# Kernel optimization log

Hardware: AMD Instinct MI355X
Metric: run time of the kernel (lower is better)

## Reference

```python
import jax, jax.numpy as jnp
import numpy as np


def setup_inputs() -> dict:
    key = jax.random.key(0)
    k1, k2, k3, k4, k5 = jax.random.split(key, 5)
    B, T, H, E, F = 4, 2048, 2048, 8, 1024
    s_h = 1.0 / np.sqrt(H)
    s_f = 1.0 / np.sqrt(F)
    return {
        "hidden_states": jax.random.normal(k1, (B, T, H), dtype=jnp.float32),
        "W_router": jax.random.normal(k2, (H, E), dtype=jnp.float32) * s_h,
        "W_gate": jax.random.normal(k3, (E, H, F), dtype=jnp.float32) * s_h,
        "W_up": jax.random.normal(k4, (E, H, F), dtype=jnp.float32) * s_h,
        "W_down": jax.random.normal(k5, (E, F, H), dtype=jnp.float32) * s_f,
    }


def reference(hidden_states, W_router, W_gate, W_up, W_down):
    B, T, H = hidden_states.shape
    E = W_router.shape[1]
    x = hidden_states.reshape(-1, H)  # [N, H]
    # ReMoE router: linear -> ReLU, non-negative weights per expert
    weights = jax.nn.relu(x @ W_router)  # [N, E]
    # Per-expert SwiGLU FFN applied to all tokens; zero-weight experts
    # contribute exactly zero, matching the original masked dispatch.
    gate = jnp.einsum('nh,ehf->enf', x, W_gate)  # [E, N, F]
    up = jnp.einsum('nh,ehf->enf', x, W_up)      # [E, N, F]
    hid = jax.nn.silu(gate) * up                 # [E, N, F]
    expert_out = jnp.einsum('enf,efh->enh', hid, W_down)  # [E, N, H]
    out_flat = jnp.einsum('ne,enh->nh', weights, expert_out)  # [N, H]
    out = out_flat.reshape(B, T, H)
    router_weights = weights.reshape(B, T, E)
    return (out, router_weights)
```

## Files before the change

### kernel.cpp

```cpp
#include <hip/hip_runtime.h>
#include <hip/hip_bf16.h>

#define N_TOK 8192
#define HD    2048
#define NE    8
#define FF    1024

using f32x4  = __attribute__((ext_vector_type(4))) float;
using bf16x8 = __attribute__((ext_vector_type(8))) __bf16;

__device__ __forceinline__ unsigned short f2bf(float f) {
  unsigned u = __float_as_uint(f);
  u += 0x7FFFu + ((u >> 16) & 1u);
  return (unsigned short)(u >> 16);
}

__device__ __forceinline__ void gl_lds16(const void* g, void* l) {
  __builtin_amdgcn_global_load_lds((__attribute__((address_space(1))) void*)g,
                                   (__attribute__((address_space(3))) void*)l,
                                   16, 0, 0);
}

__device__ __forceinline__ void stage256(const unsigned short* g, size_t lda, int k0,
                                         char* slotbase, int wv, int sr8, int scol) {
  #pragma unroll
  for (int c = 0; c < 4; ++c) {
    const int grp = c * 8 + wv;
    gl_lds16(g + (size_t)(grp * 8 + sr8) * lda + k0 + scol, slotbase + grp * 1024);
  }
}
__device__ __forceinline__ void stage256i(const unsigned short* const aP[4], int k0,
                                          char* slotbase, int wv) {
  #pragma unroll
  for (int c = 0; c < 4; ++c) {
    const int grp = c * 8 + wv;
    gl_lds16(aP[c] + k0, slotbase + grp * 1024);
  }
}
__device__ __forceinline__ void stage128(const unsigned short* g, size_t lda, int k0,
                                         char* slotbase, int wv, int sr8, int scol) {
  #pragma unroll
  for (int c = 0; c < 2; ++c) {
    const int grp = c * 8 + wv;
    gl_lds16(g + (size_t)(grp * 8 + sr8) * lda + k0 + scol, slotbase + grp * 1024);
  }
}

__global__ void k_tconv(const float* __restrict__ in, unsigned short* __restrict__ out,
                        int R, int C, size_t in_z, size_t out_z, size_t ostride) {
  __shared__ float tile[32][33];
  const int z = blockIdx.z;
  const int c0 = blockIdx.x * 32, r0 = blockIdx.y * 32;
  const int tx = threadIdx.x, ty = threadIdx.y;
  const float* ip = in + (size_t)z * in_z;
  unsigned short* op = out + (size_t)z * out_z;
  #pragma unroll
  for (int i = ty; i < 32; i += 8)
    tile[i][tx] = ip[(size_t)(r0 + i) * C + (c0 + tx)];
  __syncthreads();
  #pragma unroll
  for (int i = ty; i < 32; i += 8)
    op[(size_t)(c0 + i) * ostride + (r0 + tx)] = f2bf(tile[tx][i]);
}

__global__ void k_router(const float* __restrict__ x, const float* __restrict__ Wr,
                         float* __restrict__ w, float* __restrict__ rout,
                         unsigned short* __restrict__ xb) {
  const int lane = threadIdx.x & 63, wv = threadIdx.x >> 6;
  const int n = blockIdx.x * 4 + wv;
  const float* xr = x + (size_t)n * HD + lane * 32;
  unsigned short* xbr = xb + (size_t)n * HD + lane * 32;
  const float* wbase = Wr + (size_t)lane * 32 * NE;
  float acc[8];
  #pragma unroll
  for (int e = 0; e < 8; ++e) acc[e] = 0.f;
  #pragma unroll
  for (int kk = 0; kk < 32; kk += 4) {
    float4 xv = *reinterpret_cast<const float4*>(xr + kk);
    ushort4 o;
    o.x = f2bf(xv.x); o.y = f2bf(xv.y); o.z = f2bf(xv.z); o.w = f2bf(xv.w);
    *reinterpret_cast<ushort4*>(xbr + kk) = o;
    #pragma unroll
    for (int t = 0; t < 4; ++t) {
      const float* wrow = wbase + (kk + t) * 8;
      float4 w0 = *reinterpret_cast<const float4*>(wrow);
      float4 w1 = *reinterpret_cast<const float4*>(wrow + 4);
      float xs = (t == 0) ? xv.x : (t == 1) ? xv.y : (t == 2) ? xv.z : xv.w;
      acc[0] += xs * w0.x; acc[1] += xs * w0.y; acc[2] += xs * w0.z; acc[3] += xs * w0.w;
      acc[4] += xs * w1.x; acc[5] += xs * w1.y; acc[6] += xs * w1.z; acc[7] += xs * w1.w;
    }
  }
  #pragma unroll
  for (int off = 32; off; off >>= 1) {
    #pragma unroll
    for (int e = 0; e < 8; ++e) acc[e] += __shfl_down(acc[e], off);
  }
  if (lane == 0) {
    #pragma unroll
    for (int e = 0; e < 8; ++e) {
      float v = acc[e] > 0.f ? acc[e] : 0.f;
      w[n * 8 + e] = v;
      rout[n * 8 + e] = v;
    }
  }
}

__global__ void k_compact(const float* __restrict__ w, int* __restrict__ idx,
                          int* __restrict__ cnt) {
  const int e = blockIdx.x;
  __shared__ int base;
  __shared__ int scan[4];
  if (threadIdx.x == 0) base = 0;
  __syncthreads();
  const int lane = threadIdx.x & 63, wvi = threadIdx.x >> 6;
  for (int c0 = 0; c0 < N_TOK; c0 += 256) {
    const int n = c0 + threadIdx.x;
    const bool act = w[n * 8 + e] > 0.f;
    unsigned long long m = __ballot(act);
    const int pre  = __popcll(m & ((1ull << lane) - 1ull));
    if (lane == 0) scan[wvi] = __popcll(m);
    __syncthreads();
    int woff = 0;
    #pragma unroll
    for (int i = 0; i < 4; ++i) if (i < wvi) woff += scan[i];
    const int tot = scan[0] + scan[1] + scan[2] + scan[3];
    if (act) idx[e * N_TOK + base + woff + pre] = n;
    __syncthreads();
    if (threadIdx.x == 0) base += tot;
    __syncthreads();
  }
  const int M = base;
  if (threadIdx.x == 0) cnt[e] = M;
  const int Mpad = (M + 255) & ~255;
  for (int i = M + threadIdx.x; i < Mpad; i += 256) idx[e * N_TOK + i] = 0;
}

#define G1_PHASE(cpK) do {                                                       \
    const char* Ab_ = As + rs * 32768 + (wr * 64) * 128 + rb;                    \
    const char* Bg_ = Bgs + rs * 16384 + (wc * 64) * 128 + rb;                   \
    const char* Bu_ = Bus + rs * 16384 + (wc * 64) * 128 + rb;                   \
    bf16x8 av_[4], bg_[4], bu_[4];                                               \
    _Pragma("unroll")                                                            \
    for (int i = 0; i < 4; ++i) av_[i] = *(const bf16x8*)(Ab_ + i * 2048 + (cpK)); \
    _Pragma("unroll")                                                            \
    for (int j = 0; j < 4; ++j) {                                                \
      bg_[j] = *(const bf16x8*)(Bg_ + j * 2048 + (cpK));                         \
      bu_[j] = *(const bf16x8*)(Bu_ + j * 2048 + (cpK));                         \
    }                                                                            \
    __builtin_amdgcn_s_setprio(1);                                               \
    _Pragma("unroll")                                                            \
    for (int i = 0; i < 4; ++i) {                                                \
      _Pragma("unroll")                                                          \
      for (int j = 0; j < 4; ++j) {                                              \
        ag[i][j] = __builtin_amdgcn_mfma_f32_16x16x32_bf16(av_[i], bg_[j], ag[i][j], 0,0,0); \
        au[i][j] = __builtin_amdgcn_mfma_f32_16x16x32_bf16(av_[i], bu_[j], au[i][j], 0,0,0); \
      }                                                                          \
    }                                                                            \
    __builtin_amdgcn_s_setprio(0);                                               \
  } while (0)

__global__ void __launch_bounds__(512, 2) k_gemm1(
    const unsigned short* __restrict__ xb,
    const unsigned short* __restrict__ Wg,
    const unsigned short* __restrict__ Wu,
    const float* __restrict__ w,
    const int* __restrict__ idx,
    const int* __restrict__ cnt,
    unsigned short* __restrict__ A2,
    int e0, int k2g, int nwg) {
  extern __shared__ char lds[];
  char* As  = lds;
  char* Bgs = lds + 65536;
  char* Bus = lds + 98304;
  const int tid = threadIdx.x;
  const int l = tid & 63, wv = tid >> 6;

  const int h = blockIdx.x;
  const int chunk = nwg >> 3;
  const int L = (h & 7) * chunk + (h >> 3);
  const int eloc = L >> 8;
  const int e = e0 + eloc;
  const int idxq = L & 255;
  const int sub = idxq >> 5;
  const int f = ((sub & 1) << 2) | ((idxq >> 3) & 3);
  const int y = ((sub >> 1) << 3) | (idxq & 7);
  const int bm = y << 8;
  const int bf = f << 7;
  const int wr = wv >> 1, wc = wv & 1;

  const int Me = cnt[e];
  if (bm >= Me) return;
  const int* idxe = idx + e * N_TOK;

  const unsigned short* gBg = Wg + ((size_t)e * FF + bf) * HD;
  const unsigned short* gBu = Wu + ((size_t)e * FF + bf) * HD;

  const int sr8  = l >> 3;
  const int scol = ((l & 7) ^ sr8) << 3;
  const int fr  = l & 15;
  const int rb  = fr << 7;
  const int kc  = (l >> 4) << 4;
  const int swz = (l & 7) << 4;
  const int cp0 = kc ^ swz;
  const int cp1 = (64 + kc) ^ swz;

  const unsigned short* aP[4];
  #pragma unroll
  for (int c = 0; c < 4; ++c)
    aP[c] = xb + (size_t)idxe[bm + (c * 8 + wv) * 8 + sr8] * HD + scol;

  f32x4 ag[4][4], au[4][4];
  const f32x4 zero = {0.f, 0.f, 0.f, 0.f};
  #pragma unroll
  for (int i = 0; i < 4; ++i) {
    #pragma unroll
    for (int j = 0; j < 4; ++j) { ag[i][j] = zero; au[i][j] = zero; }
  }

  stage256i(aP, 0, As, wv);
  stage128(gBg, HD, 0, Bgs, wv, sr8, scol);
  stage128(gBu, HD, 0, Bus, wv, sr8, scol);
  asm volatile("s_waitcnt vmcnt(0)" ::: "memory");
  __builtin_amdgcn_s_barrier();
  __builtin_amdgcn_sched_barrier(0);

  const int NT = HD / 64;
  for (int t = 0; t < NT; ++t) {
    const int tn = (t + 1 < NT) ? t + 1 : NT - 1;
    const int sw = (t + 1) & 1;
    const int rs = t & 1;
    stage128(gBg, HD, tn * 64, Bgs + sw * 16384, wv, sr8, scol);
    stage128(gBu, HD, tn * 64, Bus + sw * 16384, wv, sr8, scol);
    G1_PHASE(cp0);
    stage256i(aP, tn * 64, As + sw * 32768, wv);
    G1_PHASE(cp1);
    asm volatile("s_waitcnt vmcnt(0)" ::: "memory");
    __builtin_amdgcn_s_barrier();
    __builtin_amdgcn_sched_barrier(0);
  }

  const int orow = (l >> 4) << 2;
  #pragma unroll
  for (int am = 0; am < 4; ++am) {
    #pragma unroll
    for (int rr = 0; rr < 4; ++rr) {
      const int cm = bm + wr * 64 + am * 16 + orow + rr;
      const int n = idxe[cm];
      const float wn = w[n * 8 + e];
      size_t obase = (size_t)n * k2g + (size_t)eloc * FF + bf + wc * 64 + fr;
      #pragma unroll
      for (int j = 0; j < 4; ++j) {
        const float g = ag[am][j][rr];
        const float u = au[am][j][rr];
        const float s = g / (1.f + __expf(-g));
        A2[obase + j * 16] = f2bf(s * u * wn);
      }
    }
  }
}

#define G2_PHASE(cpK) do {                                                       \
    const char* Ab_ = As + rs * 32768 + (wr * 128) * 128 + rb;                   \
    const char* Bb_ = Bs + rs * 32768 + (wc * 64) * 128 + rb;                    \
    bf16x8 av_[8], bv_[4];                                                       \
    _Pragma("unroll")                                                            \
    for (int i = 0; i < 8; ++i) av_[i] = *(const bf16x8*)(Ab_ + i * 2048 + (cpK)); \
    _Pragma("unroll")                                                            \
    for (int j = 0; j < 4; ++j) bv_[j] = *(const bf16x8*)(Bb_ + j * 2048 + (cpK)); \
    __builtin_amdgcn_s_setprio(1);                                               \
    _Pragma("unroll")                                                            \
    for (int i = 0; i < 8; ++i) {                                                \
      _Pragma("unroll")                                                          \
      for (int j = 0; j < 4; ++j)                                                \
        acc[i][j] = __builtin_amdgcn_mfma_f32_16x16x32_bf16(av_[i], bv_[j], acc[i][j], 0,0,0); \
    }                                                                            \
    __builtin_amdgcn_s_setprio(0);                                               \
  } while (0)

__global__ void __launch_bounds__(512, 2) k_gemm2(
    const unsigned short* __restrict__ A2,
    const unsigned short* __restrict__ Wd,
    float* __restrict__ out,
    int k2g, int accum) {
  extern __shared__ char lds[];
  char* As = lds;
  char* Bs = lds + 65536;
  const int tid = threadIdx.x;
  const int l = tid & 63, wv = tid >> 6;

  const int h = blockIdx.x;
  const int L = (h & 7) * 32 + (h >> 3);
  const int y = L >> 3;
  const int x = L & 7;
  const int bm = y << 8;
  const int bn = x << 8;
  const int wr = wv >> 2, wc = wv & 3;

  const unsigned short* gA = A2 + (size_t)bm * k2g;
  const unsigned short* gB = Wd + (size_t)bn * (NE * FF);

  const int sr8  = l >> 3;
  const int scol = ((l & 7) ^ sr8) << 3;
  const int fr  = l & 15;
  const int rb  = fr << 7;
  const int kc  = (l >> 4) << 4;
  const int swz = (l & 7) << 4;
  const int cp0 = kc ^ swz;
  const int cp1 = (64 + kc) ^ swz;

  f32x4 acc[8][4];
  const f32x4 zero = {0.f, 0.f, 0.f, 0.f};
  #pragma unroll
  for (int i = 0; i < 8; ++i) {
    #pragma unroll
    for (int j = 0; j < 4; ++j) acc[i][j] = zero;
  }

  stage256(gA, k2g, 0, As, wv, sr8, scol);
  stage256(gB, NE * FF, 0, Bs, wv, sr8, scol);
  asm volatile("s_waitcnt vmcnt(0)" ::: "memory");
  __builtin_amdgcn_s_barrier();
  __builtin_amdgcn_sched_barrier(0);

  const int NT = k2g / 64;
  for (int t = 0; t < NT; ++t) {
    const int tn = (t + 1 < NT) ? t + 1 : NT - 1;
    const int sw = (t + 1) & 1;
    const int rs = t & 1;
    stage256(gB, NE * FF, tn * 64, Bs + sw * 32768, wv, sr8, scol);
    G2_PHASE(cp0);
    stage256(gA, k2g, tn * 64, As + sw * 32768, wv, sr8, scol);
    G2_PHASE(cp1);
    asm volatile("s_waitcnt vmcnt(0)" ::: "memory");
    __builtin_amdgcn_s_barrier();
    __builtin_amdgcn_sched_barrier(0);
  }

  const int orow = (l >> 4) << 2;
  #pragma unroll
  for (int am = 0; am < 8; ++am) {
    #pragma unroll
    for (int rr = 0; rr < 4; ++rr) {
      const int n = bm + wr * 128 + am * 16 + orow + rr;
      float* op = out + (size_t)n * HD + bn + wc * 64 + fr;
      #pragma unroll
      for (int j = 0; j < 4; ++j) {
        const float v = acc[am][j][rr];
        op[j * 16] = accum ? (op[j * 16] + v) : v;
      }
    }
  }
}

extern "C" void kernel_launch(void* const* d_in, const int* in_sizes, int n_in,
                              void* d_out, int out_size, void* d_ws, size_t ws_size,
                              hipStream_t stream) {
  (void)in_sizes; (void)out_size;
  if (n_in < 5) return;
  const float* x  = (const float*)d_in[0];
  const float* Wr = (const float*)d_in[1];
  const float* Wg = (const float*)d_in[2];
  const float* Wu = (const float*)d_in[3];
  const float* Wd = (const float*)d_in[4];
  float* out  = (float*)d_out;
  float* rout = out + (size_t)N_TOK * HD;

  hipFuncSetAttribute((const void*)k_gemm1, hipFuncAttributeMaxDynamicSharedMemorySize, 131072);
  hipFuncSetAttribute((const void*)k_gemm2, hipFuncAttributeMaxDynamicSharedMemorySize, 131072);

  char* ws = (char*)d_ws;
  const size_t SZ_XB = (size_t)N_TOK * HD * 2;
  const size_t SZ_W  = (size_t)NE * HD * FF * 2;
  unsigned short* xb    = (unsigned short*)(ws);
  unsigned short* Wg_bt = (unsigned short*)(ws + SZ_XB);
  unsigned short* Wu_bt = (unsigned short*)(ws + SZ_XB + SZ_W);
  unsigned short* Wd_bt = (unsigned short*)(ws + SZ_XB + 2 * SZ_W);
  float*          wbuf  = (float*)(ws + SZ_XB + 3 * SZ_W);
  size_t off = SZ_XB + 3 * SZ_W + (size_t)N_TOK * NE * 4;
  int* idxbuf = (int*)(ws + off);  off += (size_t)NE * N_TOK * 4;
  int* cntbuf = (int*)(ws + off);  off += 256;
  const size_t fixed = off;
  unsigned short* A2 = (unsigned short*)(ws + fixed);

  const size_t perE = (size_t)N_TOK * FF * 2;
  int G = 8;
  while (G > 1 && fixed + (size_t)G * perE > ws_size) G >>= 1;

  dim3 tb(32, 8);
  k_tconv<<<dim3(FF / 32, HD / 32, NE), tb, 0, stream>>>(
      Wg, Wg_bt, HD, FF, (size_t)HD * FF, (size_t)FF * HD, (size_t)HD);
  k_tconv<<<dim3(FF / 32, HD / 32, NE), tb, 0, stream>>>(
      Wu, Wu_bt, HD, FF, (size_t)HD * FF, (size_t)FF * HD, (size_t)HD);
  k_tconv<<<dim3(HD / 32, FF / 32, NE), tb, 0, stream>>>(
      Wd, Wd_bt, FF, HD, (size_t)FF * HD, (size_t)FF, (size_t)(NE * FF));

  k_router<<<N_TOK / 4, 256, 0, stream>>>(x, Wr, wbuf, rout, xb);

  k_compact<<<NE, 256, 0, stream>>>(wbuf, idxbuf, cntbuf);

  const int k2g = G * FF;
  for (int e0 = 0; e0 < NE; e0 += G) {
    hipMemsetAsync(A2, 0, (size_t)G * perE, stream);
    const int nwg1 = 256 * G;
    k_gemm1<<<nwg1, 512, 131072, stream>>>(xb, Wg_bt, Wu_bt, wbuf, idxbuf, cntbuf,
                                           A2, e0, k2g, nwg1);
    k_gemm2<<<(N_TOK / 256) * (HD / 256), 512, 131072, stream>>>(
        A2, Wd_bt + (size_t)e0 * FF, out, k2g, e0 != 0);
  }
}
```

Before: 690.4 us.

## Split K tiles into halves with deeper async prefetch and partial waits in both GEMMs

Both expert GEMM kernels now stage each 64-wide K tile as two 32-wide halves in a new swizzled LDS layout. Prefetch runs up to two half-tiles ahead, and the full vmcnt(0) drain is replaced by vmcnt(8) waits with a barrier per half. Global-to-LDS loads are interleaved between MFMA groups to keep more memory traffic in flight and shorten stalls at each barrier. The cost is a second barrier per K step and more intricate buffer-reuse ordering, where a wrong wait count or slot overlap would give a race.

```diff
diff --git a/kernel.cpp b/kernel.cpp
--- a/kernel.cpp
+++ b/kernel.cpp
@@ -21,30 +21,11 @@
                                    16, 0, 0);
 }
 
-__device__ __forceinline__ void stage256(const unsigned short* g, size_t lda, int k0,
-                                         char* slotbase, int wv, int sr8, int scol) {
-  #pragma unroll
-  for (int c = 0; c < 4; ++c) {
-    const int grp = c * 8 + wv;
-    gl_lds16(g + (size_t)(grp * 8 + sr8) * lda + k0 + scol, slotbase + grp * 1024);
-  }
-}
-__device__ __forceinline__ void stage256i(const unsigned short* const aP[4], int k0,
-                                          char* slotbase, int wv) {
-  #pragma unroll
-  for (int c = 0; c < 4; ++c) {
-    const int grp = c * 8 + wv;
-    gl_lds16(aP[c] + k0, slotbase + grp * 1024);
-  }
-}
-__device__ __forceinline__ void stage128(const unsigned short* g, size_t lda, int k0,
-                                         char* slotbase, int wv, int sr8, int scol) {
-  #pragma unroll
-  for (int c = 0; c < 2; ++c) {
-    const int grp = c * 8 + wv;
-    gl_lds16(g + (size_t)(grp * 8 + sr8) * lda + k0 + scol, slotbase + grp * 1024);
-  }
-}
+#define WAIT8_BAR() do {                                      \
+    asm volatile("s_waitcnt vmcnt(8)" ::: "memory");          \
+    __builtin_amdgcn_s_barrier();                             \
+    __builtin_amdgcn_sched_barrier(0);                        \
+  } while (0)
 
 __global__ void k_tconv(const float* __restrict__ in, unsigned short* __restrict__ out,
                         int R, int C, size_t in_z, size_t out_z, size_t ostride) {
@@ -135,28 +116,40 @@
   for (int i = M + threadIdx.x; i < Mpad; i += 256) idx[e * N_TOK + i] = 0;
 }
 
-#define G1_PHASE(cpK) do {                                                       \
-    const char* Ab_ = As + rs * 32768 + (wr * 64) * 128 + rb;                    \
-    const char* Bg_ = Bgs + rs * 16384 + (wc * 64) * 128 + rb;                   \
-    const char* Bu_ = Bus + rs * 16384 + (wc * 64) * 128 + rb;                   \
-    bf16x8 av_[4], bg_[4], bu_[4];                                               \
-    _Pragma("unroll")                                                            \
-    for (int i = 0; i < 4; ++i) av_[i] = *(const bf16x8*)(Ab_ + i * 2048 + (cpK)); \
-    _Pragma("unroll")                                                            \
-    for (int j = 0; j < 4; ++j) {                                                \
-      bg_[j] = *(const bf16x8*)(Bg_ + j * 2048 + (cpK));                         \
-      bu_[j] = *(const bf16x8*)(Bu_ + j * 2048 + (cpK));                         \
-    }                                                                            \
+#define G1_MFMA(accM, barr) do {                                                 \
     __builtin_amdgcn_s_setprio(1);                                               \
     _Pragma("unroll")                                                            \
     for (int i = 0; i < 4; ++i) {                                                \
       _Pragma("unroll")                                                          \
-      for (int j = 0; j < 4; ++j) {                                              \
-        ag[i][j] = __builtin_amdgcn_mfma_f32_16x16x32_bf16(av_[i], bg_[j], ag[i][j], 0,0,0); \
-        au[i][j] = __builtin_amdgcn_mfma_f32_16x16x32_bf16(av_[i], bu_[j], au[i][j], 0,0,0); \
-      }                                                                          \
+      for (int j = 0; j < 4; ++j)                                                \
+        accM[i][j] = __builtin_amdgcn_mfma_f32_16x16x32_bf16(av_[i], (barr)[j], accM[i][j], 0,0,0); \
     }                                                                            \
     __builtin_amdgcn_s_setprio(0);                                               \
+  } while (0)
+
+#define G1_ST_A(koff, base) do {                                                 \
+    gl_lds16(aP0 + (koff), (base) + wv * 1024);                                  \
+    gl_lds16(aP1 + (koff), (base) + (wv + 8) * 1024);                            \
+  } while (0)
+#define G1_ST_B(koff, bgb, bub) do {                                             \
+    gl_lds16(gBg + bOff + (koff), (bgb) + wv * 1024);                            \
+    gl_lds16(gBu + bOff + (koff), (bub) + wv * 1024);                            \
+  } while (0)
+
+#define G1_HALF(rsl, hh, ISSUE_B) do {                                           \
+    const char* Ab_ = As  + (rsl) * 32768 + (hh) * 16384 + aoff;                 \
+    const char* Bg_ = Bgs + (rsl) * 16384 + (hh) * 8192 + boff;                  \
+    const char* Bu_ = Bus + (rsl) * 16384 + (hh) * 8192 + boff;                  \
+    bf16x8 av_[4], bb_[4];                                                       \
+    _Pragma("unroll")                                                            \
+    for (int i = 0; i < 4; ++i) av_[i] = *(const bf16x8*)(Ab_ + i * 1024);       \
+    _Pragma("unroll")                                                            \
+    for (int j = 0; j < 4; ++j) bb_[j] = *(const bf16x8*)(Bg_ + j * 1024);       \
+    G1_MFMA(ag, bb_);                                                            \
+    ISSUE_B;                                                                     \
+    _Pragma("unroll")                                                            \
+    for (int j = 0; j < 4; ++j) bb_[j] = *(const bf16x8*)(Bu_ + j * 1024);       \
+    G1_MFMA(au, bb_);                                                            \
   } while (0)
 
 __global__ void __launch_bounds__(512, 2) k_gemm1(
@@ -195,19 +188,15 @@
   const unsigned short* gBg = Wg + ((size_t)e * FF + bf) * HD;
   const unsigned short* gBu = Wu + ((size_t)e * FF + bf) * HD;
 
-  const int sr8  = l >> 3;
-  const int scol = ((l & 7) ^ sr8) << 3;
+  const int scolE = (((l & 3) ^ ((l >> 3) & 3)) << 3);
   const int fr  = l & 15;
-  const int rb  = fr << 7;
-  const int kc  = (l >> 4) << 4;
-  const int swz = (l & 7) << 4;
-  const int cp0 = kc ^ swz;
-  const int cp1 = (64 + kc) ^ swz;
-
-  const unsigned short* aP[4];
-  #pragma unroll
-  for (int c = 0; c < 4; ++c)
-    aP[c] = xb + (size_t)idxe[bm + (c * 8 + wv) * 8 + sr8] * HD + scol;
+  const int cph = (((l >> 4) ^ ((fr >> 1) & 3)) << 4);
+  const int aoff = (wr * 64 + fr) * 64 + cph;
+  const int boff = (wc * 64 + fr) * 64 + cph;
+
+  const unsigned short* aP0 = xb + (size_t)idxe[bm + wv * 16 + (l >> 2)] * HD + scolE;
+  const unsigned short* aP1 = xb + (size_t)idxe[bm + (wv + 8) * 16 + (l >> 2)] * HD + scolE;
+  const size_t bOff = (size_t)(wv * 16 + (l >> 2)) * HD + scolE;
 
   f32x4 ag[4][4], au[4][4];
   const f32x4 zero = {0.f, 0.f, 0.f, 0.f};
@@ -217,26 +206,25 @@
     for (int j = 0; j < 4; ++j) { ag[i][j] = zero; au[i][j] = zero; }
   }
 
-  stage256i(aP, 0, As, wv);
-  stage128(gBg, HD, 0, Bgs, wv, sr8, scol);
-  stage128(gBu, HD, 0, Bus, wv, sr8, scol);
-  asm volatile("s_waitcnt vmcnt(0)" ::: "memory");
-  __builtin_amdgcn_s_barrier();
-  __builtin_amdgcn_sched_barrier(0);
+  G1_ST_A(0,  As);
+  G1_ST_B(0,  Bgs, Bus);
+  G1_ST_A(32, As + 16384);
+  G1_ST_B(32, Bgs + 8192, Bus + 8192);
+  G1_ST_A(64, As + 32768);
+  G1_ST_B(64, Bgs + 16384, Bus + 16384);
+  WAIT8_BAR();
 
   const int NT = HD / 64;
   for (int t = 0; t < NT; ++t) {
-    const int tn = (t + 1 < NT) ? t + 1 : NT - 1;
-    const int sw = (t + 1) & 1;
-    const int rs = t & 1;
-    stage128(gBg, HD, tn * 64, Bgs + sw * 16384, wv, sr8, scol);
-    stage128(gBu, HD, tn * 64, Bus + sw * 16384, wv, sr8, scol);
-    G1_PHASE(cp0);
-    stage256i(aP, tn * 64, As + sw * 32768, wv);
-    G1_PHASE(cp1);
-    asm volatile("s_waitcnt vmcnt(0)" ::: "memory");
-    __builtin_amdgcn_s_barrier();
-    __builtin_amdgcn_sched_barrier(0);
+    const int rs = t & 1, sw = rs ^ 1;
+    const int kn1 = ((t + 1 < NT) ? t + 1 : NT - 1) * 64;
+    const int kn2 = ((t + 2 < NT) ? t + 2 : NT - 1) * 64;
+    G1_ST_A(kn1 + 32, As + sw * 32768 + 16384);
+    G1_HALF(rs, 0, G1_ST_B(kn1 + 32, Bgs + sw * 16384 + 8192, Bus + sw * 16384 + 8192));
+    WAIT8_BAR();
+    G1_ST_A(kn2, As + rs * 32768);
+    G1_HALF(rs, 1, G1_ST_B(kn2, Bgs + rs * 16384, Bus + rs * 16384));
+    WAIT8_BAR();
   }
 
   const int orow = (l >> 4) << 2;
@@ -259,17 +247,35 @@
   }
 }
 
-#define G2_PHASE(cpK) do {                                                       \
-    const char* Ab_ = As + rs * 32768 + (wr * 128) * 128 + rb;                   \
-    const char* Bb_ = Bs + rs * 32768 + (wc * 64) * 128 + rb;                    \
+#define G2_ST_A(koff, base) do {                                                 \
+    gl_lds16(gA + aOff0 + (koff), (base) + wv * 1024);                           \
+    gl_lds16(gA + aOff1 + (koff), (base) + (wv + 8) * 1024);                     \
+  } while (0)
+#define G2_ST_B(koff, base) do {                                                 \
+    gl_lds16(gB + bOff0 + (koff), (base) + wv * 1024);                           \
+    gl_lds16(gB + bOff1 + (koff), (base) + (wv + 8) * 1024);                     \
+  } while (0)
+
+#define G2_HALF(rsl, hh, ISSUE_B) do {                                           \
+    const char* Ab_ = As + (rsl) * 32768 + (hh) * 16384 + aoff;                  \
+    const char* Bb_ = Bs + (rsl) * 32768 + (hh) * 16384 + boff;                  \
     bf16x8 av_[8], bv_[4];                                                       \
     _Pragma("unroll")                                                            \
-    for (int i = 0; i < 8; ++i) av_[i] = *(const bf16x8*)(Ab_ + i * 2048 + (cpK)); \
-    _Pragma("unroll")                                                            \
-    for (int j = 0; j < 4; ++j) bv_[j] = *(const bf16x8*)(Bb_ + j * 2048 + (cpK)); \
+    for (int i = 0; i < 8; ++i) av_[i] = *(const bf16x8*)(Ab_ + i * 1024);       \
+    _Pragma("unroll")                                                            \
+    for (int j = 0; j < 4; ++j) bv_[j] = *(const bf16x8*)(Bb_ + j * 1024);       \
     __builtin_amdgcn_s_setprio(1);                                               \
     _Pragma("unroll")                                                            \
-    for (int i = 0; i < 8; ++i) {                                                \
+    for (int i = 0; i < 4; ++i) {                                                \
+      _Pragma("unroll")                                                          \
+      for (int j = 0; j < 4; ++j)                                                \
+        acc[i][j] = __builtin_amdgcn_mfma_f32_16x16x32_bf16(av_[i], bv_[j], acc[i][j], 0,0,0); \
+    }                                                                            \
+    __builtin_amdgcn_s_setprio(0);                                               \
+    ISSUE_B;                                                                     \
+    __builtin_amdgcn_s_setprio(1);                                               \
+    _Pragma("unroll")                                                            \
+    for (int i = 4; i < 8; ++i) {                                                \
       _Pragma("unroll")                                                          \
       for (int j = 0; j < 4; ++j)                                                \
         acc[i][j] = __builtin_amdgcn_mfma_f32_16x16x32_bf16(av_[i], bv_[j], acc[i][j], 0,0,0); \
@@ -299,14 +305,16 @@
   const unsigned short* gA = A2 + (size_t)bm * k2g;
   const unsigned short* gB = Wd + (size_t)bn * (NE * FF);
 
-  const int sr8  = l >> 3;
-  const int scol = ((l & 7) ^ sr8) << 3;
+  const int scolE = (((l & 3) ^ ((l >> 3) & 3)) << 3);
   const int fr  = l & 15;
-  const int rb  = fr << 7;
-  const int kc  = (l >> 4) << 4;
-  const int swz = (l & 7) << 4;
-  const int cp0 = kc ^ swz;
-  const int cp1 = (64 + kc) ^ swz;
+  const int cph = (((l >> 4) ^ ((fr >> 1) & 3)) << 4);
+  const int aoff = (wr * 128 + fr) * 64 + cph;
+  const int boff = (wc * 64 + fr) * 64 + cph;
+
+  const size_t aOff0 = (size_t)(wv * 16 + (l >> 2)) * k2g + scolE;
+  const size_t aOff1 = (size_t)((wv + 8) * 16 + (l >> 2)) * k2g + scolE;
+  const size_t bOff0 = (size_t)(wv * 16 + (l >> 2)) * (NE * FF) + scolE;
+  const size_t bOff1 = (size_t)((wv + 8) * 16 + (l >> 2)) * (NE * FF) + scolE;
 
   f32x4 acc[8][4];
   const f32x4 zero = {0.f, 0.f, 0.f, 0.f};
@@ -316,24 +324,25 @@
     for (int j = 0; j < 4; ++j) acc[i][j] = zero;
   }
 
-  stage256(gA, k2g, 0, As, wv, sr8, scol);
-  stage256(gB, NE * FF, 0, Bs, wv, sr8, scol);
-  asm volatile("s_waitcnt vmcnt(0)" ::: "memory");
-  __builtin_amdgcn_s_barrier();
-  __builtin_amdgcn_sched_barrier(0);
+  G2_ST_A(0,  As);
+  G2_ST_B(0,  Bs);
+  G2_ST_A(32, As + 16384);
+  G2_ST_B(32, Bs + 16384);
+  G2_ST_A(64, As + 32768);
+  G2_ST_B(64, Bs + 32768);
+  WAIT8_BAR();
 
   const int NT = k2g / 64;
   for (int t = 0; t < NT; ++t) {
-    const int tn = (t + 1 < NT) ? t + 1 : NT - 1;
-    const int sw = (t + 1) & 1;
-    const int rs = t & 1;
-    stage256(gB, NE * FF, tn * 64, Bs + sw * 32768, wv, sr8, scol);
-    G2_PHASE(cp0);
-    stage256(gA, k2g, tn * 64, As + sw * 32768, wv, sr8, scol);
-    G2_PHASE(cp1);
-    asm volatile("s_waitcnt vmcnt(0)" ::: "memory");
-    __builtin_amdgcn_s_barrier();
-    __builtin_amdgcn_sched_barrier(0);
+    const int rs = t & 1, sw = rs ^ 1;
+    const int kn1 = ((t + 1 < NT) ? t + 1 : NT - 1) * 64;
+    const int kn2 = ((t + 2 < NT) ? t + 2 : NT - 1) * 64;
+    G2_ST_A(kn1 + 32, As + sw * 32768 + 16384);
+    G2_HALF(rs, 0, G2_ST_B(kn1 + 32, Bs + sw * 32768 + 16384));
+    WAIT8_BAR();
+    G2_ST_A(kn2, As + rs * 32768);
+    G2_HALF(rs, 1, G2_ST_B(kn2, Bs + rs * 32768));
+    WAIT8_BAR();
   }
 
   const int orow = (l >> 4) << 2;
```

Result: slower. 710.3 us (+2.9%).

## Restructure GEMM main loops into barrier-phased ping-pong with finer load/MFMA interleave

Applied to the files above, without the earlier changes.

Both expert GEMM kernels now split each K-tile into four barrier-separated phases. Each phase issues a slice of global-to-LDS prefetch and then runs a block of MFMAs, and partial vmcnt waits replace the full drain at the end of every iteration. Staging is reorganised so each thread loads contiguous 16-byte chunks by thread id, LDS reads use a new swizzle, and the gate and up products share one B register set in turn. gemm1 also drops its grouped tile-to-block mapping in favour of a plain f/y split. The changes aim to overlap memory traffic with matrix math, at the cost of more barriers and more ordering-sensitive code.

```diff
diff --git a/kernel.cpp b/kernel.cpp
--- a/kernel.cpp
+++ b/kernel.cpp
@@ -9,6 +9,10 @@
 using f32x4  = __attribute__((ext_vector_type(4))) float;
 using bf16x8 = __attribute__((ext_vector_type(8))) __bf16;
 
+#define MFMA16(a, b, c) __builtin_amdgcn_mfma_f32_16x16x32_bf16((a), (b), (c), 0, 0, 0)
+#define BARX() do { __builtin_amdgcn_s_barrier(); __builtin_amdgcn_sched_barrier(0); } while (0)
+#define VMW(N) asm volatile("s_waitcnt vmcnt(" #N ")" ::: "memory")
+
 __device__ __forceinline__ unsigned short f2bf(float f) {
   unsigned u = __float_as_uint(f);
   u += 0x7FFFu + ((u >> 16) & 1u);
@@ -19,31 +23,6 @@
   __builtin_amdgcn_global_load_lds((__attribute__((address_space(1))) void*)g,
                                    (__attribute__((address_space(3))) void*)l,
                                    16, 0, 0);
-}
-
-__device__ __forceinline__ void stage256(const unsigned short* g, size_t lda, int k0,
-                                         char* slotbase, int wv, int sr8, int scol) {
-  #pragma unroll
-  for (int c = 0; c < 4; ++c) {
-    const int grp = c * 8 + wv;
-    gl_lds16(g + (size_t)(grp * 8 + sr8) * lda + k0 + scol, slotbase + grp * 1024);
-  }
-}
-__device__ __forceinline__ void stage256i(const unsigned short* const aP[4], int k0,
-                                          char* slotbase, int wv) {
-  #pragma unroll
-  for (int c = 0; c < 4; ++c) {
-    const int grp = c * 8 + wv;
-    gl_lds16(aP[c] + k0, slotbase + grp * 1024);
-  }
-}
-__device__ __forceinline__ void stage128(const unsigned short* g, size_t lda, int k0,
-                                         char* slotbase, int wv, int sr8, int scol) {
-  #pragma unroll
-  for (int c = 0; c < 2; ++c) {
-    const int grp = c * 8 + wv;
-    gl_lds16(g + (size_t)(grp * 8 + sr8) * lda + k0 + scol, slotbase + grp * 1024);
-  }
 }
 
 __global__ void k_tconv(const float* __restrict__ in, unsigned short* __restrict__ out,
@@ -135,26 +114,14 @@
   for (int i = M + threadIdx.x; i < Mpad; i += 256) idx[e * N_TOK + i] = 0;
 }
 
-#define G1_PHASE(cpK) do {                                                       \
-    const char* Ab_ = As + rs * 32768 + (wr * 64) * 128 + rb;                    \
-    const char* Bg_ = Bgs + rs * 16384 + (wc * 64) * 128 + rb;                   \
-    const char* Bu_ = Bus + rs * 16384 + (wc * 64) * 128 + rb;                   \
-    bf16x8 av_[4], bg_[4], bu_[4];                                               \
-    _Pragma("unroll")                                                            \
-    for (int i = 0; i < 4; ++i) av_[i] = *(const bf16x8*)(Ab_ + i * 2048 + (cpK)); \
+#define G1_MM(p, ACC) do {                                                       \
+    __builtin_amdgcn_s_setprio(1);                                               \
     _Pragma("unroll")                                                            \
     for (int j = 0; j < 4; ++j) {                                                \
-      bg_[j] = *(const bf16x8*)(Bg_ + j * 2048 + (cpK));                         \
-      bu_[j] = *(const bf16x8*)(Bu_ + j * 2048 + (cpK));                         \
-    }                                                                            \
-    __builtin_amdgcn_s_setprio(1);                                               \
-    _Pragma("unroll")                                                            \
-    for (int i = 0; i < 4; ++i) {                                                \
-      _Pragma("unroll")                                                          \
-      for (int j = 0; j < 4; ++j) {                                              \
-        ag[i][j] = __builtin_amdgcn_mfma_f32_16x16x32_bf16(av_[i], bg_[j], ag[i][j], 0,0,0); \
-        au[i][j] = __builtin_amdgcn_mfma_f32_16x16x32_bf16(av_[i], bu_[j], au[i][j], 0,0,0); \
-      }                                                                          \
+      ACC[(p)*2][j]   = MFMA16(av_[(p)*2][0],   b_[j][0], ACC[(p)*2][j]);        \
+      ACC[(p)*2][j]   = MFMA16(av_[(p)*2][1],   b_[j][1], ACC[(p)*2][j]);        \
+      ACC[(p)*2+1][j] = MFMA16(av_[(p)*2+1][0], b_[j][0], ACC[(p)*2+1][j]);      \
+      ACC[(p)*2+1][j] = MFMA16(av_[(p)*2+1][1], b_[j][1], ACC[(p)*2+1][j]);      \
     }                                                                            \
     __builtin_amdgcn_s_setprio(0);                                               \
   } while (0)
@@ -181,9 +148,8 @@
   const int eloc = L >> 8;
   const int e = e0 + eloc;
   const int idxq = L & 255;
-  const int sub = idxq >> 5;
-  const int f = ((sub & 1) << 2) | ((idxq >> 3) & 3);
-  const int y = ((sub >> 1) << 3) | (idxq & 7);
+  const int f = idxq >> 5;
+  const int y = idxq & 31;
   const int bm = y << 8;
   const int bf = f << 7;
   const int wr = wv >> 1, wc = wv & 1;
@@ -195,19 +161,19 @@
   const unsigned short* gBg = Wg + ((size_t)e * FF + bf) * HD;
   const unsigned short* gBu = Wu + ((size_t)e * FF + bf) * HD;
 
-  const int sr8  = l >> 3;
-  const int scol = ((l & 7) ^ sr8) << 3;
+  const int scolE = ((tid & 7) ^ ((tid >> 3) & 7)) << 3;
   const int fr  = l & 15;
-  const int rb  = fr << 7;
-  const int kc  = (l >> 4) << 4;
-  const int swz = (l & 7) << 4;
-  const int cp0 = kc ^ swz;
-  const int cp1 = (64 + kc) ^ swz;
-
-  const unsigned short* aP[4];
+  const int cph0 = (((l >> 4) ^ (l & 7)) << 4);
+  const int cph1 = (((4 + (l >> 4)) ^ (l & 7)) << 4);
+
+  const unsigned short* aQ[4];
   #pragma unroll
   for (int c = 0; c < 4; ++c)
-    aP[c] = xb + (size_t)idxe[bm + (c * 8 + wv) * 8 + sr8] * HD + scol;
+    aQ[c] = xb + (size_t)idxe[bm + c * 64 + (tid >> 3)] * HD + scolE;
+  size_t srcW[2];
+  #pragma unroll
+  for (int c = 0; c < 2; ++c)
+    srcW[c] = (size_t)(c * 64 + (tid >> 3)) * HD + scolE;
 
   f32x4 ag[4][4], au[4][4];
   const f32x4 zero = {0.f, 0.f, 0.f, 0.f};
@@ -217,26 +183,72 @@
     for (int j = 0; j < 4; ++j) { ag[i][j] = zero; au[i][j] = zero; }
   }
 
-  stage256i(aP, 0, As, wv);
-  stage128(gBg, HD, 0, Bgs, wv, sr8, scol);
-  stage128(gBu, HD, 0, Bus, wv, sr8, scol);
-  asm volatile("s_waitcnt vmcnt(0)" ::: "memory");
-  __builtin_amdgcn_s_barrier();
-  __builtin_amdgcn_sched_barrier(0);
+  gl_lds16(aQ[0], As + 0 * 8192 + tid * 16);
+  gl_lds16(aQ[1], As + 1 * 8192 + tid * 16);
+  gl_lds16(aQ[2], As + 2 * 8192 + tid * 16);
+  gl_lds16(aQ[3], As + 3 * 8192 + tid * 16);
+  gl_lds16(gBg + srcW[0], Bgs + 0 * 8192 + tid * 16);
+  gl_lds16(gBg + srcW[1], Bgs + 1 * 8192 + tid * 16);
+  gl_lds16(gBu + srcW[0], Bus + 0 * 8192 + tid * 16);
+  gl_lds16(gBu + srcW[1], Bus + 1 * 8192 + tid * 16);
+  VMW(2);
+  BARX();
 
   const int NT = HD / 64;
   for (int t = 0; t < NT; ++t) {
-    const int tn = (t + 1 < NT) ? t + 1 : NT - 1;
-    const int sw = (t + 1) & 1;
-    const int rs = t & 1;
-    stage128(gBg, HD, tn * 64, Bgs + sw * 16384, wv, sr8, scol);
-    stage128(gBu, HD, tn * 64, Bus + sw * 16384, wv, sr8, scol);
-    G1_PHASE(cp0);
-    stage256i(aP, tn * 64, As + sw * 32768, wv);
-    G1_PHASE(cp1);
-    asm volatile("s_waitcnt vmcnt(0)" ::: "memory");
-    __builtin_amdgcn_s_barrier();
-    __builtin_amdgcn_sched_barrier(0);
+    const int rs = t & 1, sd = rs ^ 1;
+    const int kn = ((t + 1 < NT) ? t + 1 : NT - 1) * 64;
+    const char* Ar = As + rs * 32768;
+    const char* Gr = Bgs + rs * 16384;
+    const char* Ur = Bus + rs * 16384;
+    char* Ad = As + sd * 32768;
+    char* Gd = Bgs + sd * 16384;
+    char* Ud = Bus + sd * 16384;
+    bf16x8 av_[4][2], b_[4][2];
+    {
+      const char* Ab_ = Ar + (wr * 64 + fr) * 128;
+      #pragma unroll
+      for (int m = 0; m < 4; ++m) {
+        av_[m][0] = *(const bf16x8*)(Ab_ + m * 2048 + cph0);
+        av_[m][1] = *(const bf16x8*)(Ab_ + m * 2048 + cph1);
+      }
+      const char* Gb_ = Gr + (wc * 64 + fr) * 128;
+      #pragma unroll
+      for (int j = 0; j < 4; ++j) {
+        b_[j][0] = *(const bf16x8*)(Gb_ + j * 2048 + cph0);
+        b_[j][1] = *(const bf16x8*)(Gb_ + j * 2048 + cph1);
+      }
+    }
+    gl_lds16(aQ[0] + kn, Ad + 0 * 8192 + tid * 16);
+    gl_lds16(aQ[1] + kn, Ad + 1 * 8192 + tid * 16);
+    BARX();
+    G1_MM(0, ag);
+    BARX();
+    gl_lds16(aQ[2] + kn, Ad + 2 * 8192 + tid * 16);
+    gl_lds16(aQ[3] + kn, Ad + 3 * 8192 + tid * 16);
+    BARX();
+    G1_MM(1, ag);
+    VMW(4);
+    BARX();
+    {
+      const char* Ub_ = Ur + (wc * 64 + fr) * 128;
+      #pragma unroll
+      for (int j = 0; j < 4; ++j) {
+        b_[j][0] = *(const bf16x8*)(Ub_ + j * 2048 + cph0);
+        b_[j][1] = *(const bf16x8*)(Ub_ + j * 2048 + cph1);
+      }
+    }
+    gl_lds16(gBg + srcW[0] + kn, Gd + 0 * 8192 + tid * 16);
+    gl_lds16(gBg + srcW[1] + kn, Gd + 1 * 8192 + tid * 16);
+    BARX();
+    G1_MM(0, au);
+    BARX();
+    gl_lds16(gBu + srcW[0] + kn, Ud + 0 * 8192 + tid * 16);
+    gl_lds16(gBu + srcW[1] + kn, Ud + 1 * 8192 + tid * 16);
+    BARX();
+    G1_MM(1, au);
+    VMW(2);
+    BARX();
   }
 
   const int orow = (l >> 4) << 2;
@@ -259,20 +271,22 @@
   }
 }
 
-#define G2_PHASE(cpK) do {                                                       \
-    const char* Ab_ = As + rs * 32768 + (wr * 128) * 128 + rb;                   \
-    const char* Bb_ = Bs + rs * 32768 + (wc * 64) * 128 + rb;                    \
-    bf16x8 av_[8], bv_[4];                                                       \
-    _Pragma("unroll")                                                            \
-    for (int i = 0; i < 8; ++i) av_[i] = *(const bf16x8*)(Ab_ + i * 2048 + (cpK)); \
-    _Pragma("unroll")                                                            \
-    for (int j = 0; j < 4; ++j) bv_[j] = *(const bf16x8*)(Bb_ + j * 2048 + (cpK)); \
+#define G2_RD_A(p) do {                                                          \
+    const char* Ab_ = Ar + (wr * 128 + (p) * 32 + fr) * 128;                     \
+    av_[0][0] = *(const bf16x8*)(Ab_ + cph0);                                    \
+    av_[0][1] = *(const bf16x8*)(Ab_ + cph1);                                    \
+    av_[1][0] = *(const bf16x8*)(Ab_ + 2048 + cph0);                             \
+    av_[1][1] = *(const bf16x8*)(Ab_ + 2048 + cph1);                             \
+  } while (0)
+
+#define G2_MM(p) do {                                                            \
     __builtin_amdgcn_s_setprio(1);                                               \
     _Pragma("unroll")                                                            \
-    for (int i = 0; i < 8; ++i) {                                                \
-      _Pragma("unroll")                                                          \
-      for (int j = 0; j < 4; ++j)                                                \
-        acc[i][j] = __builtin_amdgcn_mfma_f32_16x16x32_bf16(av_[i], bv_[j], acc[i][j], 0,0,0); \
+    for (int j = 0; j < 4; ++j) {                                                \
+      acc[(p)*2][j]   = MFMA16(av_[0][0], bv_[j][0], acc[(p)*2][j]);             \
+      acc[(p)*2][j]   = MFMA16(av_[0][1], bv_[j][1], acc[(p)*2][j]);             \
+      acc[(p)*2+1][j] = MFMA16(av_[1][0], bv_[j][0], acc[(p)*2+1][j]);           \
+      acc[(p)*2+1][j] = MFMA16(av_[1][1], bv_[j][1], acc[(p)*2+1][j]);           \
     }                                                                            \
     __builtin_amdgcn_s_setprio(0);                                               \
   } while (0)
@@ -299,14 +313,17 @@
   const unsigned short* gA = A2 + (size_t)bm * k2g;
   const unsigned short* gB = Wd + (size_t)bn * (NE * FF);
 
-  const int sr8  = l >> 3;
-  const int scol = ((l & 7) ^ sr8) << 3;
+  const int scolE = ((tid & 7) ^ ((tid >> 3) & 7)) << 3;
   const int fr  = l & 15;
-  const int rb  = fr << 7;
-  const int kc  = (l >> 4) << 4;
-  const int swz = (l & 7) << 4;
-  const int cp0 = kc ^ swz;
-  const int cp1 = (64 + kc) ^ swz;
+  const int cph0 = (((l >> 4) ^ (l & 7)) << 4);
+  const int cph1 = (((4 + (l >> 4)) ^ (l & 7)) << 4);
+
+  size_t srcA[4], srcB[4];
+  #pragma unroll
+  for (int c = 0; c < 4; ++c) {
+    srcA[c] = (size_t)(c * 64 + (tid >> 3)) * k2g + scolE;
+    srcB[c] = (size_t)(c * 64 + (tid >> 3)) * (NE * FF) + scolE;
+  }
 
   f32x4 acc[8][4];
   const f32x4 zero = {0.f, 0.f, 0.f, 0.f};
@@ -316,24 +333,60 @@
     for (int j = 0; j < 4; ++j) acc[i][j] = zero;
   }
 
-  stage256(gA, k2g, 0, As, wv, sr8, scol);
-  stage256(gB, NE * FF, 0, Bs, wv, sr8, scol);
-  asm volatile("s_waitcnt vmcnt(0)" ::: "memory");
-  __builtin_amdgcn_s_barrier();
-  __builtin_amdgcn_sched_barrier(0);
+  gl_lds16(gB + srcB[0], Bs + 0 * 8192 + tid * 16);
+  gl_lds16(gB + srcB[1], Bs + 1 * 8192 + tid * 16);
+  gl_lds16(gB + srcB[2], Bs + 2 * 8192 + tid * 16);
+  gl_lds16(gB + srcB[3], Bs + 3 * 8192 + tid * 16);
+  gl_lds16(gA + srcA[0], As + 0 * 8192 + tid * 16);
+  gl_lds16(gA + srcA[2], As + 2 * 8192 + tid * 16);
+  gl_lds16(gA + srcA[1], As + 1 * 8192 + tid * 16);
+  gl_lds16(gA + srcA[3], As + 3 * 8192 + tid * 16);
+  VMW(2);
+  BARX();
 
   const int NT = k2g / 64;
   for (int t = 0; t < NT; ++t) {
-    const int tn = (t + 1 < NT) ? t + 1 : NT - 1;
-    const int sw = (t + 1) & 1;
-    const int rs = t & 1;
-    stage256(gB, NE * FF, tn * 64, Bs + sw * 32768, wv, sr8, scol);
-    G2_PHASE(cp0);
-    stage256(gA, k2g, tn * 64, As + sw * 32768, wv, sr8, scol);
-    G2_PHASE(cp1);
-    asm volatile("s_waitcnt vmcnt(0)" ::: "memory");
-    __builtin_amdgcn_s_barrier();
-    __builtin_amdgcn_sched_barrier(0);
+    const int rs = t & 1, sd = rs ^ 1;
+    const int kn = ((t + 1 < NT) ? t + 1 : NT - 1) * 64;
+    const char* Ar = As + rs * 32768;
+    const char* Br = Bs + rs * 32768;
+    char* Ad = As + sd * 32768;
+    char* Bd = Bs + sd * 32768;
+    bf16x8 bv_[4][2], av_[2][2];
+    {
+      const char* Bb_ = Br + (wc * 64 + fr) * 128;
+      #pragma unroll
+      for (int j = 0; j < 4; ++j) {
+        bv_[j][0] = *(const bf16x8*)(Bb_ + j * 2048 + cph0);
+        bv_[j][1] = *(const bf16x8*)(Bb_ + j * 2048 + cph1);
+      }
+    }
+    G2_RD_A(0);
+    gl_lds16(gB + srcB[0] + kn, Bd + 0 * 8192 + tid * 16);
+    gl_lds16(gB + srcB[1] + kn, Bd + 1 * 8192 + tid * 16);
+    BARX();
+    G2_MM(0);
+    BARX();
+    G2_RD_A(1);
+    gl_lds16(gB + srcB[2] + kn, Bd + 2 * 8192 + tid * 16);
+    gl_lds16(gB + srcB[3] + kn, Bd + 3 * 8192 + tid * 16);
+    BARX();
+    G2_MM(1);
+    VMW(4);
+    BARX();
+    G2_RD_A(2);
+    gl_lds16(gA + srcA[0] + kn, Ad + 0 * 8192 + tid * 16);
+    gl_lds16(gA + srcA[2] + kn, Ad + 2 * 8192 + tid * 16);
+    BARX();
+    G2_MM(2);
+    BARX();
+    G2_RD_A(3);
+    gl_lds16(gA + srcA[1] + kn, Ad + 1 * 8192 + tid * 16);
+    gl_lds16(gA + srcA[3] + kn, Ad + 3 * 8192 + tid * 16);
+    BARX();
+    G2_MM(3);
+    VMW(2);
+    BARX();
   }
 
   const int orow = (l >> 4) << 2;
```

Result: no change. 700.7 us (+1.5%).

## Make down-projection sparse per expert with compacted rows and gather-combine

Applied to the files above, without the earlier changes.

GEMM1 now writes its SwiGLU outputs into per-expert compacted rows instead of a dense token-by-expert scatter. A new per-expert GEMM2 skips row tiles beyond each expert's active count and writes into a per-expert output buffer. A gather kernel then sums each token's active expert rows into the final output, using a reverse index built during compaction. This drops the A2 memset and the dense down-projection over inactive tokens, but adds a large fp32 intermediate (8×N×H) plus an extra read/write pass. It needs enough workspace, otherwise the old path runs.

```diff
diff --git a/kernel.cpp b/kernel.cpp
--- a/kernel.cpp
+++ b/kernel.cpp
@@ -106,7 +106,7 @@
 }
 
 __global__ void k_compact(const float* __restrict__ w, int* __restrict__ idx,
-                          int* __restrict__ cnt) {
+                          int* __restrict__ rev, int* __restrict__ cnt) {
   const int e = blockIdx.x;
   __shared__ int base;
   __shared__ int scan[4];
@@ -124,7 +124,9 @@
     #pragma unroll
     for (int i = 0; i < 4; ++i) if (i < wvi) woff += scan[i];
     const int tot = scan[0] + scan[1] + scan[2] + scan[3];
-    if (act) idx[e * N_TOK + base + woff + pre] = n;
+    const int pos = base + woff + pre;
+    if (act) idx[e * N_TOK + pos] = n;
+    rev[n * NE + e] = act ? pos : -1;
     __syncthreads();
     if (threadIdx.x == 0) base += tot;
     __syncthreads();
@@ -167,7 +169,7 @@
     const int* __restrict__ idx,
     const int* __restrict__ cnt,
     unsigned short* __restrict__ A2,
-    int e0, int k2g, int nwg) {
+    int e0, int k2g, int nwg, int compacted) {
   extern __shared__ char lds[];
   char* As  = lds;
   char* Bgs = lds + 65536;
@@ -247,7 +249,11 @@
       const int cm = bm + wr * 64 + am * 16 + orow + rr;
       const int n = idxe[cm];
       const float wn = w[n * 8 + e];
-      size_t obase = (size_t)n * k2g + (size_t)eloc * FF + bf + wc * 64 + fr;
+      size_t obase;
+      if (compacted)
+        obase = (size_t)eloc * N_TOK * FF + (size_t)cm * FF + bf + wc * 64 + fr;
+      else
+        obase = (size_t)n * k2g + (size_t)eloc * FF + bf + wc * 64 + fr;
       #pragma unroll
       for (int j = 0; j < 4; ++j) {
         const float g = ag[am][j][rr];
@@ -352,6 +358,104 @@
   }
 }
 
+__global__ void __launch_bounds__(512, 2) k_gemm2s(
+    const unsigned short* __restrict__ A2c,
+    const unsigned short* __restrict__ Wd,
+    const int* __restrict__ cnt,
+    float* __restrict__ outc) {
+  extern __shared__ char lds[];
+  char* As = lds;
+  char* Bs = lds + 65536;
+  const int tid = threadIdx.x;
+  const int l = tid & 63, wv = tid >> 6;
+
+  const int h = blockIdx.x;
+  const int L = (h & 7) * 256 + (h >> 3);
+  const int eloc = L >> 8;
+  const int idxq = L & 255;
+  const int x = idxq >> 5;
+  const int y = idxq & 31;
+  const int bm = y << 8;
+  const int bn = x << 8;
+  const int wr = wv >> 2, wc = wv & 3;
+
+  const int Me = cnt[eloc];
+  if (bm >= Me) return;
+
+  const unsigned short* gA = A2c + (size_t)eloc * N_TOK * FF + (size_t)bm * FF;
+  const unsigned short* gB = Wd + (size_t)bn * (NE * FF) + (size_t)eloc * FF;
+
+  const int sr8  = l >> 3;
+  const int scol = ((l & 7) ^ sr8) << 3;
+  const int fr  = l & 15;
+  const int rb  = fr << 7;
+  const int kc  = (l >> 4) << 4;
+  const int swz = (l & 7) << 4;
+  const int cp0 = kc ^ swz;
+  const int cp1 = (64 + kc) ^ swz;
+
+  f32x4 acc[8][4];
+  const f32x4 zero = {0.f, 0.f, 0.f, 0.f};
+  #pragma unroll
+  for (int i = 0; i < 8; ++i) {
+    #pragma unroll
+    for (int j = 0; j < 4; ++j) acc[i][j] = zero;
+  }
+
+  stage256(gA, FF, 0, As, wv, sr8, scol);
+  stage256(gB, NE * FF, 0, Bs, wv, sr8, scol);
+  asm volatile("s_waitcnt vmcnt(0)" ::: "memory");
+  __builtin_amdgcn_s_barrier();
+  __builtin_amdgcn_sched_barrier(0);
+
+  const int NT = FF / 64;
+  for (int t = 0; t < NT; ++t) {
+    const int tn = (t + 1 < NT) ? t + 1 : NT - 1;
+    const int sw = (t + 1) & 1;
+    const int rs = t & 1;
+    stage256(gB, NE * FF, tn * 64, Bs + sw * 32768, wv, sr8, scol);
+    G2_PHASE(cp0);
+    stage256(gA, FF, tn * 64, As + sw * 32768, wv, sr8, scol);
+    G2_PHASE(cp1);
+    asm volatile("s_waitcnt vmcnt(0)" ::: "memory");
+    __builtin_amdgcn_s_barrier();
+    __builtin_amdgcn_sched_barrier(0);
+  }
+
+  float* oce = outc + (size_t)eloc * N_TOK * HD;
+  const int orow = (l >> 4) << 2;
+  #pragma unroll
+  for (int am = 0; am < 8; ++am) {
+    #pragma unroll
+    for (int rr = 0; rr < 4; ++rr) {
+      const int cm = bm + wr * 128 + am * 16 + orow + rr;
+      float* op = oce + (size_t)cm * HD + bn + wc * 64 + fr;
+      #pragma unroll
+      for (int j = 0; j < 4; ++j) op[j * 16] = acc[am][j][rr];
+    }
+  }
+}
+
+__global__ void k_gather(const float* __restrict__ outc, const int* __restrict__ rev,
+                         float* __restrict__ out) {
+  const int n = blockIdx.x;
+  const int h0 = threadIdx.x * 8;
+  float4 a0 = {0.f, 0.f, 0.f, 0.f}, a1 = {0.f, 0.f, 0.f, 0.f};
+  #pragma unroll
+  for (int e = 0; e < NE; ++e) {
+    const int cm = rev[n * NE + e];
+    if (cm >= 0) {
+      const float4* p = reinterpret_cast<const float4*>(
+          outc + (size_t)e * N_TOK * HD + (size_t)cm * HD + h0);
+      float4 v0 = p[0], v1 = p[1];
+      a0.x += v0.x; a0.y += v0.y; a0.z += v0.z; a0.w += v0.w;
+      a1.x += v1.x; a1.y += v1.y; a1.z += v1.z; a1.w += v1.w;
+    }
+  }
+  float4* op = reinterpret_cast<float4*>(out + (size_t)n * HD + h0);
+  op[0] = a0; op[1] = a1;
+}
+
 extern "C" void kernel_launch(void* const* d_in, const int* in_sizes, int n_in,
                               void* d_out, int out_size, void* d_ws, size_t ws_size,
                               hipStream_t stream) {
@@ -365,8 +469,9 @@
   float* out  = (float*)d_out;
   float* rout = out + (size_t)N_TOK * HD;
 
-  hipFuncSetAttribute((const void*)k_gemm1, hipFuncAttributeMaxDynamicSharedMemorySize, 131072);
-  hipFuncSetAttribute((const void*)k_gemm2, hipFuncAttributeMaxDynamicSharedMemorySize, 131072);
+  hipFuncSetAttribute((const void*)k_gemm1,  hipFuncAttributeMaxDynamicSharedMemorySize, 131072);
+  hipFuncSetAttribute((const void*)k_gemm2,  hipFuncAttributeMaxDynamicSharedMemorySize, 131072);
+  hipFuncSetAttribute((const void*)k_gemm2s, hipFuncAttributeMaxDynamicSharedMemorySize, 131072);
 
   char* ws = (char*)d_ws;
   const size_t SZ_XB = (size_t)N_TOK * HD * 2;
@@ -378,13 +483,17 @@
   float*          wbuf  = (float*)(ws + SZ_XB + 3 * SZ_W);
   size_t off = SZ_XB + 3 * SZ_W + (size_t)N_TOK * NE * 4;
   int* idxbuf = (int*)(ws + off);  off += (size_t)NE * N_TOK * 4;
+  int* revbuf = (int*)(ws + off);  off += (size_t)NE * N_TOK * 4;
   int* cntbuf = (int*)(ws + off);  off += 256;
   const size_t fixed = off;
   unsigned short* A2 = (unsigned short*)(ws + fixed);
 
   const size_t perE = (size_t)N_TOK * FF * 2;
-  int G = 8;
-  while (G > 1 && fixed + (size_t)G * perE > ws_size) G >>= 1;
+  const size_t SZ_A2   = (size_t)NE * perE;
+  const size_t SZ_OUTC = (size_t)NE * N_TOK * HD * 4;
+  float* outc = (float*)(ws + fixed + SZ_A2);
+
+  const bool sparse2 = (ws_size >= fixed + SZ_A2 + SZ_OUTC);
 
   dim3 tb(32, 8);
   k_tconv<<<dim3(FF / 32, HD / 32, NE), tb, 0, stream>>>(
@@ -396,15 +505,25 @@
 
   k_router<<<N_TOK / 4, 256, 0, stream>>>(x, Wr, wbuf, rout, xb);
 
-  k_compact<<<NE, 256, 0, stream>>>(wbuf, idxbuf, cntbuf);
-
-  const int k2g = G * FF;
-  for (int e0 = 0; e0 < NE; e0 += G) {
-    hipMemsetAsync(A2, 0, (size_t)G * perE, stream);
-    const int nwg1 = 256 * G;
+  k_compact<<<NE, 256, 0, stream>>>(wbuf, idxbuf, revbuf, cntbuf);
+
+  if (sparse2) {
+    const int nwg1 = 256 * NE;
     k_gemm1<<<nwg1, 512, 131072, stream>>>(xb, Wg_bt, Wu_bt, wbuf, idxbuf, cntbuf,
-                                           A2, e0, k2g, nwg1);
-    k_gemm2<<<(N_TOK / 256) * (HD / 256), 512, 131072, stream>>>(
-        A2, Wd_bt + (size_t)e0 * FF, out, k2g, e0 != 0);
-  }
-}
+                                           A2, 0, NE * FF, nwg1, 1);
+    k_gemm2s<<<2048, 512, 131072, stream>>>(A2, Wd_bt, cntbuf, outc);
+    k_gather<<<N_TOK, 256, 0, stream>>>(outc, revbuf, out);
+  } else {
+    int G = 8;
+    while (G > 1 && fixed + (size_t)G * perE > ws_size) G >>= 1;
+    const int k2g = G * FF;
+    for (int e0 = 0; e0 < NE; e0 += G) {
+      hipMemsetAsync(A2, 0, (size_t)G * perE, stream);
+      const int nwg1 = 256 * G;
+      k_gemm1<<<nwg1, 512, 131072, stream>>>(xb, Wg_bt, Wu_bt, wbuf, idxbuf, cntbuf,
+                                             A2, e0, k2g, nwg1, 0);
+      k_gemm2<<<(N_TOK / 256) * (HD / 256), 512, 131072, stream>>>(
+          A2, Wd_bt + (size_t)e0 * FF, out, k2g, e0 != 0);
+    }
+  }
+}
```

Measured after the change: 699.3 us. Within noise of the previous version (+1.3%).
